# Optimization experiments

Measured on AMD Instinct MI355X. Metric: run time of the kernel, lower is better.

The kernel has to match this reference:

```python
import jax, jax.numpy as jnp
import numpy as np

H = 12        # num attention heads
W = 256       # one-sided window (attention_window // 2)
NEG = -1e9    # additive mask value


def setup_inputs() -> dict:
    key = jax.random.key(0)
    ks = jax.random.split(key, 6)
    B, S, D = 2, 4096, 768
    inp = {
        "hidden_states": jax.random.normal(ks[0], (B, S, D), dtype=jnp.float32),
        "attention_mask": jnp.zeros((B, S), dtype=jnp.float32),
        "Wq": jax.random.normal(ks[1], (D, D), dtype=jnp.float32) * 0.02,
        "bq": jnp.zeros((D,), dtype=jnp.float32),
        "Wk": jax.random.normal(ks[2], (D, D), dtype=jnp.float32) * 0.02,
        "bk": jnp.zeros((D,), dtype=jnp.float32),
        "Wv": jax.random.normal(ks[3], (D, D), dtype=jnp.float32) * 0.02,
        "bv": jnp.zeros((D,), dtype=jnp.float32),
        "Wo": jax.random.normal(ks[4], (D, D), dtype=jnp.float32) * 0.02,
        "bo": jnp.zeros((D,), dtype=jnp.float32),
    }
    return inp


def _sliding_window_attn(hidden_states, attention_mask, Wq, bq, Wk, bk, Wv, bv, Wo, bo):
    B, S, D = hidden_states.shape
    dh = D // H
    b = W                 # chunk size == one-sided window
    nb = S // b           # number of chunks (S must be multiple of W)

    # projections; Longformer scales the query by 1/sqrt(d_head)
    q = (hidden_states @ Wq.T + bq) / jnp.sqrt(jnp.float32(dh))
    k = hidden_states @ Wk.T + bk
    v = hidden_states @ Wv.T + bv

    # [B, H, S, dh]
    q = q.reshape(B, S, H, dh).transpose(0, 2, 1, 3)
    k = k.reshape(B, S, H, dh).transpose(0, 2, 1, 3)
    v = v.reshape(B, S, H, dh).transpose(0, 2, 1, 3)

    # chunk queries: [B, H, nb, b, dh]
    qb = q.reshape(B, H, nb, b, dh)

    # pad K/V by one chunk on each side, gather 3 consecutive chunks per query chunk
    kp = jnp.pad(k, ((0, 0), (0, 0), (b, b), (0, 0)))
    vp = jnp.pad(v, ((0, 0), (0, 0), (b, b), (0, 0)))
    idx = jnp.arange(nb)[:, None] * b + jnp.arange(3 * b)[None, :]  # [nb, 3b] into padded seq
    kw = kp[:, :, idx]  # [B, H, nb, 3b, dh]
    vw = vp[:, :, idx]  # [B, H, nb, 3b, dh]

    # banded scores: [B, H, nb, b, 3b]
    scores = jnp.einsum("bhnqd,bhnkd->bhnqk", qb, kw)

    # band mask: query at local pos qi (global n*b+qi) vs key at local pos ki
    # (global n*b + ki - b); relative offset = ki - b - qi, keep |offset| <= W
    rel = jnp.arange(3 * b)[None, :] - b - jnp.arange(b)[:, None]      # [b, 3b]
    band = jnp.abs(rel) <= W
    # sequence-boundary mask: key global position must lie in [0, S)
    kpos = idx - b                                                      # [nb, 3b]
    inbounds = (kpos >= 0) & (kpos < S)
    valid = band[None, :, :] & inbounds[:, None, :]                     # [nb, b, 3b]

    # key padding bias from attention_mask (wrapper passes attention_mask * -1)
    neg_mask = attention_mask * -1.0                                    # [B, S]
    mp = jnp.pad(neg_mask, ((0, 0), (b, b)))
    key_bias = mp[:, idx]                                               # [B, nb, 3b]

    scores = scores + key_bias[:, None, :, None, :]
    scores = jnp.where(valid[None, None], scores, NEG)

    probs = jax.nn.softmax(scores, axis=-1)
    ctx = jnp.einsum("bhnqk,bhnkd->bhnqd", probs, vw)                   # [B, H, nb, b, dh]
    ctx = ctx.reshape(B, H, S, dh).transpose(0, 2, 1, 3).reshape(B, S, D)

    return ctx @ Wo.T + bo


def reference(hidden_states, attention_mask, Wq, bq, Wk, bk, Wv, bv, Wo, bo):
    return _sliding_window_attn(hidden_states, attention_mask,
                                Wq, bq, Wk, bk, Wv, bv, Wo, bo)
```

## Files before the change

### kernel.cpp

```cpp
#include <hip/hip_runtime.h>
#include <hip/hip_bf16.h>
#include <stdint.h>

#define NH 12
#define DH 64
#define SEQ 4096
#define DM 768
#define NEGV -1e9f
#define LOG2E 1.4426950408889634f
#define QSCALE 0.1803368801111601f

using bf16x8 = __attribute__((ext_vector_type(8))) short;
using f32x4  = __attribute__((ext_vector_type(4))) float;

static __device__ __forceinline__ short f2bf(float f) {
  unsigned u = __builtin_bit_cast(unsigned, f);
  u += 0x7fffu + ((u >> 16) & 1u);
  return (short)(u >> 16);
}

static __device__ __forceinline__ unsigned pack2bf(float lo, float hi) {
  unsigned a = __builtin_bit_cast(unsigned, lo);
  a += 0x7fffu + ((a >> 16) & 1u);
  unsigned b = __builtin_bit_cast(unsigned, hi);
  b += 0x7fffu + ((b >> 16) & 1u);
  return (a >> 16) | (b & 0xffff0000u);
}

static __device__ __forceinline__ void gload16(const void* g, void* l) {
  __builtin_amdgcn_global_load_lds(
      (const __attribute__((address_space(1))) unsigned*)g,
      (__attribute__((address_space(3))) unsigned*)l, 16, 0, 0);
}

static __device__ __forceinline__ f32x4 mfma16(bf16x8 a, bf16x8 b, f32x4 c) {
  return __builtin_amdgcn_mfma_f32_16x16x32_bf16(a, b, c, 0, 0, 0);
}

__global__ __launch_bounds__(256) void cvt_x(const float* __restrict__ X,
                                             short* __restrict__ Xb, int n4) {
  int i = blockIdx.x * 256 + threadIdx.x;
  if (i >= n4) return;
  float4 v = ((const float4*)X)[i];
  short4 o; o.x = f2bf(v.x); o.y = f2bf(v.y); o.z = f2bf(v.z); o.w = f2bf(v.w);
  ((short4*)Xb)[i] = o;
}

__global__ __launch_bounds__(256) void cvt_w(
    const float* __restrict__ Wq, const float* __restrict__ Wk,
    const float* __restrict__ Wv, const float* __restrict__ Wo,
    short* __restrict__ Wqkv, short* __restrict__ Wob) {
  int i = blockIdx.x * 256 + threadIdx.x;
  const int n1 = 2304 * 768 / 4;
  if (i < n1) {
    int e = i * 4;
    int row = e / 768;
    const float* src;
    float sc = 1.0f;
    if (row < 768)       { src = Wq + e; sc = QSCALE; }
    else if (row < 1536) { src = Wk + e - 768 * 768; }
    else                 { src = Wv + e - 1536 * 768; }
    float4 v = *(const float4*)src;
    short4 o; o.x = f2bf(v.x * sc); o.y = f2bf(v.y * sc);
    o.z = f2bf(v.z * sc); o.w = f2bf(v.w * sc);
    ((short4*)Wqkv)[i] = o;
  } else {
    int j = i - n1;
    if (j >= 768 * 768 / 4) return;
    float4 v = ((const float4*)Wo)[j];
    short4 o; o.x = f2bf(v.x); o.y = f2bf(v.y); o.z = f2bf(v.z); o.w = f2bf(v.w);
    ((short4*)Wob)[j] = o;
  }
}

__global__ __launch_bounds__(256) void gemm_qkv(
    const short* __restrict__ Xb, const short* __restrict__ Wqkv,
    const float* __restrict__ bq, const float* __restrict__ bk,
    const float* __restrict__ bv,
    short* __restrict__ qO, short* __restrict__ kO, short* __restrict__ vT) {
  __shared__ __align__(16) short sm[128 * 132];
  short* As = sm;
  short* Bs = sm + 4096;
  const int tid = threadIdx.x, lane = tid & 63, wid = tid >> 6;
  const int m0 = blockIdx.x * 128, n0 = blockIdx.y * 128;
  const int wr = (wid >> 1) * 64, wc = (wid & 1) * 64;
  const int K = 768;
  const short* Ag = Xb + (m0 + (tid >> 2)) * K + ((tid & 3) << 3);
  const short* Bg = Wqkv + (n0 + (tid >> 2)) * K + ((tid & 3) << 3);
  short* Al = As + tid * 8;
  short* Bl = Bs + tid * 8;
  f32x4 acc[4][4] = {};
  for (int kt = 0; kt < K; kt += 32) {
    __syncthreads();
    gload16(Ag + kt, Al);
    gload16(Ag + kt + 64 * K, Al + 2048);
    gload16(Bg + kt, Bl);
    gload16(Bg + kt + 64 * K, Bl + 2048);
    __syncthreads();
    bf16x8 a[4], b[4];
#pragma unroll
    for (int mi = 0; mi < 4; ++mi)
      a[mi] = *(const bf16x8*)&As[(wr + mi * 16 + (lane & 15)) * 32 + ((lane >> 4) << 3)];
#pragma unroll
    for (int ni = 0; ni < 4; ++ni)
      b[ni] = *(const bf16x8*)&Bs[(wc + ni * 16 + (lane & 15)) * 32 + ((lane >> 4) << 3)];
#pragma unroll
    for (int mi = 0; mi < 4; ++mi)
#pragma unroll
      for (int ni = 0; ni < 4; ++ni)
        acc[mi][ni] = mfma16(a[mi], b[ni], acc[mi][ni]);
  }
  const int src = n0 / 768;
  const int bb = m0 >> 12;
  const int s0 = m0 & (SEQ - 1);
  const int nloc = n0 % 768;
  float bias[4];
#pragma unroll
  for (int ni = 0; ni < 4; ++ni) {
    int c = wc + ni * 16 + (lane & 15);
    bias[ni] = (src == 0) ? bq[nloc + c] * QSCALE
             : (src == 1) ? bk[nloc + c] : bv[nloc + c];
  }
  __syncthreads();
  if (src < 2) {
#pragma unroll
    for (int mi = 0; mi < 4; ++mi)
#pragma unroll
      for (int ni = 0; ni < 4; ++ni) {
        int row = wr + mi * 16 + ((lane >> 4) << 2);
        int col = wc + ni * 16 + (lane & 15);
#pragma unroll
        for (int r = 0; r < 4; ++r)
          sm[(row + r) * 132 + col] = f2bf(acc[mi][ni][r] + bias[ni]);
      }
    __syncthreads();
    short* dst = (src == 0) ? qO : kO;
    for (int u = tid; u < 8192; u += 256) {
      int r = u >> 6, cp = (u & 63) << 1;
      unsigned val = *(const unsigned*)&sm[r * 132 + cp];
      int c = nloc + cp;
      int h = c >> 6, d = c & 63;
      *(unsigned*)&dst[(((bb * NH + h) * SEQ) + s0 + r) * DH + d] = val;
    }
  } else {
#pragma unroll
    for (int mi = 0; mi < 4; ++mi)
#pragma unroll
      for (int ni = 0; ni < 4; ++ni) {
        int row = wr + mi * 16 + ((lane >> 4) << 2);
        int col = wc + ni * 16 + (lane & 15);
        short4 pk;
        pk.x = f2bf(acc[mi][ni][0] + bias[ni]);
        pk.y = f2bf(acc[mi][ni][1] + bias[ni]);
        pk.z = f2bf(acc[mi][ni][2] + bias[ni]);
        pk.w = f2bf(acc[mi][ni][3] + bias[ni]);
        *(short4*)&sm[col * 132 + row] = pk;
      }
    __syncthreads();
    for (int u = tid; u < 8192; u += 256) {
      int cc = u >> 6, rp = (u & 63) << 1;
      unsigned val = *(const unsigned*)&sm[cc * 132 + rp];
      int c = nloc + cc;
      int h = c >> 6, d = c & 63;
      *(unsigned*)&vT[(((bb * NH + h) * DH) + d) * SEQ + s0 + rp] = val;
    }
  }
}

__global__ __launch_bounds__(512, 4) void attn(
    const short* __restrict__ qI, const short* __restrict__ kI,
    const short* __restrict__ vT, const float* __restrict__ amask,
    short* __restrict__ ctx) {
  __shared__ __align__(16) short Ks[128 * 64];
  __shared__ __align__(16) short Vs[64 * 128];
  __shared__ __align__(16) short Ps[8][16 * 132];
  const int tid = threadIdx.x, lane = tid & 63, wid = tid >> 6;
  const int vb_id = (blockIdx.x & 7) * 96 + (blockIdx.x >> 3);
  const int strip = vb_id & 31;
  const int hh = (vb_id >> 5) % 12;
  const int bb = vb_id / 384;
  const int s0 = strip * 128;
  const int n = s0 >> 8;
  const int i0 = s0 & 255;
  const int bh = bb * NH + hh;
  const int m = lane & 15, hq = lane >> 4;
  const int swz = m & 7;
  const int iw = i0 + (wid << 4);

  const short* qbase = qI + ((size_t)(bh * SEQ) + s0 + (wid << 4)) * DH;
  const bf16x8 aq0 = *(const bf16x8*)(qbase + m * DH + (hq << 3));
  const bf16x8 aq1 = *(const bf16x8*)(qbase + m * DH + 32 + (hq << 3));

  const int kb_s0 = m * 64 + ((hq ^ swz) << 3);
  const int kb_s1 = m * 64 + (((hq + 4) ^ swz) << 3);
  const int vk0 = m * 128 + ((hq ^ swz) << 3);
  const int vk1 = m * 128 + (((hq + 4) ^ swz) << 3);
  const int vk2 = m * 128 + (((hq + 8) ^ swz) << 3);
  const int vk3 = m * 128 + (((hq + 12) ^ swz) << 3);
  short* Pw = Ps[wid];
  const int pwr = m * 132;

  const int e0 = tid * 8, e1 = tid * 8 + 4096;
  const int kj0 = e0 >> 6, kj1 = e1 >> 6;
  const int ksrc0 = kj0 * DH + ((((e0 >> 3) & 7) ^ (kj0 & 7)) << 3);
  const int ksrc1 = kj1 * DH + ((((e1 >> 3) & 7) ^ (kj1 & 7)) << 3);
  const int vd0 = e0 >> 7, vd1 = e1 >> 7;
  const int vsrc0 = vd0 * SEQ + ((((e0 >> 3) & 15) ^ (vd0 & 7)) << 3);
  const int vsrc1 = vd1 * SEQ + ((((e1 >> 3) & 15) ^ (vd1 & 7)) << 3);

  const short* kg0 = kI + (size_t)bh * SEQ * DH;
  const short* vg0 = vT + (size_t)bh * DH * SEQ;
  const float* mk0 = amask + bb * SEQ + (hq << 2);

  f32x4 acc[4] = {};
  float mrow = -1e30f, lrow = 0.f;

#pragma unroll 1
  for (int c = 0; c < 6; ++c) {
    const int j0 = c << 7;
    const int kpos0 = ((n - 1) << 8) + j0;
    if (kpos0 < 0 || kpos0 >= SEQ) continue;
    if (j0 + 127 < i0 || j0 > i0 + 639) continue;

    __syncthreads();
    {
      const short* kb = kg0 + (size_t)kpos0 * DH;
      gload16(kb + ksrc0, (short*)Ks + e0);
      gload16(kb + ksrc1, (short*)Ks + e1);
      const short* vbp = vg0 + kpos0;
      gload16(vbp + vsrc0, (short*)Vs + e0);
      gload16(vbp + vsrc1, (short*)Vs + e1);
    }
    __syncthreads();

    f32x4 sc[8];
    __builtin_amdgcn_s_setprio(1);
#pragma unroll
    for (int jt = 0; jt < 8; ++jt) {
      bf16x8 k0 = *(const bf16x8*)(Ks + jt * 1024 + kb_s0);
      bf16x8 k1 = *(const bf16x8*)(Ks + jt * 1024 + kb_s1);
      f32x4 z = {};
      z = mfma16(k0, aq0, z);
      z = mfma16(k1, aq1, z);
      sc[jt] = z;
    }
    __builtin_amdgcn_s_setprio(0);

    const float* mp = mk0 + kpos0;
    float mn = mrow;
    const bool interior = (j0 >= iw + 15) && (j0 <= iw + 385);
    if (interior) {
#pragma unroll
      for (int jt = 0; jt < 8; ++jt) {
        float4 b4 = *(const float4*)(mp + jt * 16);
#pragma unroll
        for (int r = 0; r < 4; ++r) {
          float s = fmaf(-LOG2E, (&b4.x)[r], sc[jt][r]);
          sc[jt][r] = s;
          mn = fmaxf(mn, s);
        }
      }
    } else {
      const int iq = iw + m;
#pragma unroll
      for (int jt = 0; jt < 8; ++jt) {
        float4 b4 = *(const float4*)(mp + jt * 16);
        const int jb = j0 + jt * 16 + (hq << 2);
#pragma unroll
        for (int r = 0; r < 4; ++r) {
          int j = jb + r;
          float s = fmaf(-LOG2E, (&b4.x)[r], sc[jt][r]);
          s = (j >= iq && j <= iq + 512) ? s : NEGV;
          sc[jt][r] = s;
          mn = fmaxf(mn, s);
        }
      }
    }
    mn = fmaxf(mn, __shfl_xor(mn, 16));
    mn = fmaxf(mn, __shfl_xor(mn, 32));

    float l0 = 0.f;
#pragma unroll
    for (int jt = 0; jt < 8; ++jt) {
      float p0 = exp2f(sc[jt][0] - mn);
      float p1 = exp2f(sc[jt][1] - mn);
      float p2 = exp2f(sc[jt][2] - mn);
      float p3 = exp2f(sc[jt][3] - mn);
      l0 += (p0 + p1) + (p2 + p3);
      uint2 u;
      u.x = pack2bf(p0, p1);
      u.y = pack2bf(p2, p3);
      *(uint2*)(Pw + pwr + jt * 16 + (hq << 2)) = u;
    }
    l0 += __shfl_xor(l0, 16);
    l0 += __shfl_xor(l0, 32);
    const float scl = exp2f(mrow - mn);
    lrow = lrow * scl + l0;
    mrow = mn;
    const float s0r = __shfl(scl, (hq << 2) + 0);
    const float s1r = __shfl(scl, (hq << 2) + 1);
    const float s2r = __shfl(scl, (hq << 2) + 2);
    const float s3r = __shfl(scl, (hq << 2) + 3);
#pragma unroll
    for (int nt = 0; nt < 4; ++nt) {
      acc[nt][0] *= s0r; acc[nt][1] *= s1r;
      acc[nt][2] *= s2r; acc[nt][3] *= s3r;
    }

    asm volatile("s_waitcnt lgkmcnt(0)" ::: "memory");
    __builtin_amdgcn_sched_barrier(0);

    __builtin_amdgcn_s_setprio(1);
#pragma unroll
    for (int ks = 0; ks < 4; ++ks) {
      bf16x8 pa = *(const bf16x8*)(Pw + pwr + ks * 32 + (hq << 3));
      const int vkk = (ks == 0) ? vk0 : (ks == 1) ? vk1 : (ks == 2) ? vk2 : vk3;
#pragma unroll
      for (int nt = 0; nt < 4; ++nt) {
        bf16x8 vv = *(const bf16x8*)(Vs + nt * 2048 + vkk);
        acc[nt] = mfma16(pa, vv, acc[nt]);
      }
    }
    __builtin_amdgcn_s_setprio(0);
  }

  const float inv = 1.0f / lrow;
  const float i0r = __shfl(inv, (hq << 2) + 0);
  const float i1r = __shfl(inv, (hq << 2) + 1);
  const float i2r = __shfl(inv, (hq << 2) + 2);
  const float i3r = __shfl(inv, (hq << 2) + 3);
#pragma unroll
  for (int nt = 0; nt < 4; ++nt) {
    Pw[((hq << 2) + 0) * 72 + nt * 16 + m] = f2bf(acc[nt][0] * i0r);
    Pw[((hq << 2) + 1) * 72 + nt * 16 + m] = f2bf(acc[nt][1] * i1r);
    Pw[((hq << 2) + 2) * 72 + nt * 16 + m] = f2bf(acc[nt][2] * i2r);
    Pw[((hq << 2) + 3) * 72 + nt * 16 + m] = f2bf(acc[nt][3] * i3r);
  }
  asm volatile("s_waitcnt lgkmcnt(0)" ::: "memory");
  __builtin_amdgcn_sched_barrier(0);
#pragma unroll
  for (int it = 0; it < 2; ++it) {
    int row = it * 8 + (lane >> 3);
    bf16x8 val = *(const bf16x8*)(Pw + row * 72 + ((lane & 7) << 3));
    *(bf16x8*)(ctx + ((size_t)(bb * SEQ) + s0 + (wid << 4) + row) * DM +
               hh * DH + ((lane & 7) << 3)) = val;
  }
}

__global__ __launch_bounds__(256) void gemm_out(
    const short* __restrict__ Cb, const short* __restrict__ Wob,
    const float* __restrict__ bo, float* __restrict__ out) {
  __shared__ __align__(16) short As[128 * 32];
  __shared__ __align__(16) short Bs[128 * 32];
  const int tid = threadIdx.x, lane = tid & 63, wid = tid >> 6;
  const int m0 = blockIdx.x * 128, n0 = blockIdx.y * 128;
  const int wr = (wid >> 1) * 64, wc = (wid & 1) * 64;
  const int K = 768;
  const short* Ag = Cb + (m0 + (tid >> 2)) * K + ((tid & 3) << 3);
  const short* Bg = Wob + (n0 + (tid >> 2)) * K + ((tid & 3) << 3);
  short* Al = As + tid * 8;
  short* Bl = Bs + tid * 8;
  f32x4 acc[4][4] = {};
  for (int kt = 0; kt < K; kt += 32) {
    __syncthreads();
    gload16(Ag + kt, Al);
    gload16(Ag + kt + 64 * K, Al + 2048);
    gload16(Bg + kt, Bl);
    gload16(Bg + kt + 64 * K, Bl + 2048);
    __syncthreads();
    bf16x8 a[4], b[4];
#pragma unroll
    for (int mi = 0; mi < 4; ++mi)
      a[mi] = *(const bf16x8*)&As[(wr + mi * 16 + (lane & 15)) * 32 + ((lane >> 4) << 3)];
#pragma unroll
    for (int ni = 0; ni < 4; ++ni)
      b[ni] = *(const bf16x8*)&Bs[(wc + ni * 16 + (lane & 15)) * 32 + ((lane >> 4) << 3)];
#pragma unroll
    for (int mi = 0; mi < 4; ++mi)
#pragma unroll
      for (int ni = 0; ni < 4; ++ni)
        acc[mi][ni] = mfma16(a[mi], b[ni], acc[mi][ni]);
  }
  float bias[4];
#pragma unroll
  for (int ni = 0; ni < 4; ++ni)
    bias[ni] = bo[n0 + wc + ni * 16 + (lane & 15)];
#pragma unroll
  for (int mi = 0; mi < 4; ++mi)
#pragma unroll
    for (int ni = 0; ni < 4; ++ni) {
      int row = m0 + wr + mi * 16 + ((lane >> 4) << 2);
      int col = n0 + wc + ni * 16 + (lane & 15);
#pragma unroll
      for (int r = 0; r < 4; ++r)
        out[(row + r) * DM + col] = acc[mi][ni][r] + bias[ni];
    }
}

extern "C" void kernel_launch(void* const* d_in, const int* in_sizes, int n_in,
                              void* d_out, int out_size, void* d_ws, size_t ws_size,
                              hipStream_t stream) {
  (void)in_sizes; (void)n_in; (void)out_size; (void)ws_size;
  const float* hs    = (const float*)d_in[0];
  const float* amask = (const float*)d_in[1];
  const float* Wq = (const float*)d_in[2];
  const float* bq = (const float*)d_in[3];
  const float* Wk = (const float*)d_in[4];
  const float* bk = (const float*)d_in[5];
  const float* Wv = (const float*)d_in[6];
  const float* bv = (const float*)d_in[7];
  const float* Wo = (const float*)d_in[8];
  const float* bo = (const float*)d_in[9];
  float* out = (float*)d_out;
  char* ws = (char*)d_ws;
  short* Xb   = (short*)(ws);
  short* Wqkv = (short*)(ws + 12582912);
  short* Wob  = (short*)(ws + 16121856);
  short* qB   = (short*)(ws + 17301504);
  short* kB   = (short*)(ws + 29884416);
  short* vTB  = (short*)(ws + 42467328);
  short* ctx  = Xb;

  cvt_x<<<dim3(6144), dim3(256), 0, stream>>>(hs, Xb, 8192 * 768 / 4);
  cvt_w<<<dim3(2304), dim3(256), 0, stream>>>(Wq, Wk, Wv, Wo, Wqkv, Wob);
  gemm_qkv<<<dim3(64, 18), dim3(256), 0, stream>>>(Xb, Wqkv, bq, bk, bv, qB, kB, vTB);
  attn<<<dim3(768), dim3(512), 0, stream>>>(qB, kB, vTB, amask, ctx);
  gemm_out<<<dim3(64, 6), dim3(256), 0, stream>>>(ctx, Wob, bo, out);
}
```

Measured before the change: 150.4 us.

## Pipeline both GEMMs with 4-stage LDS ring, XOR swizzle, and XCD-aware tile mapping

Replaces the single-buffered load/sync/compute loop in the QKV and output GEMMs with a four-slot LDS ring that keeps three k-tiles of global-to-LDS loads in flight. It uses explicit vmcnt waits and one barrier per iteration, and raises MFMA priority with s_setprio. The LDS column layout is XOR-swizzled to reduce bank conflicts on fragment reads. The 2D grid is flattened with an XCD-aware block-to-tile mapping so that neighbouring M tiles land on the same XCD for L2 reuse. The cost is more LDS per block (64KB), which may lower occupancy, plus fragile manual waitcnt accounting.

```diff
diff --git a/kernel.cpp b/kernel.cpp
--- a/kernel.cpp
+++ b/kernel.cpp
@@ -36,6 +36,12 @@
 static __device__ __forceinline__ f32x4 mfma16(bf16x8 a, bf16x8 b, f32x4 c) {
   return __builtin_amdgcn_mfma_f32_16x16x32_bf16(a, b, c, 0, 0, 0);
 }
+
+#define SBAR() __builtin_amdgcn_sched_barrier(0)
+#define WAIT8() asm volatile("s_waitcnt vmcnt(8)" ::: "memory")
+#define WAIT4() asm volatile("s_waitcnt vmcnt(4)" ::: "memory")
+#define WAIT0() asm volatile("s_waitcnt vmcnt(0)" ::: "memory")
+#define HBAR() __builtin_amdgcn_s_barrier()
 
 __global__ __launch_bounds__(256) void cvt_x(const float* __restrict__ X,
                                              short* __restrict__ Xb, int n4) {
@@ -73,54 +79,80 @@
   }
 }
 
+#define GEMM_PIPELINE(SM, AG, BG, ACC, LANE, WR, WC)                           \
+  {                                                                            \
+    const int l15 = (LANE) & 15, gw = (LANE) >> 4;                             \
+    const int s_ = (l15 >> 1) & 3;                                             \
+    const int fcol = ((gw ^ s_) << 3);                                         \
+    const int NT = 24;                                             \
+    auto stage = [&](int t) {                                                  \
+      short* ab = (SM) + ((t & 3) << 12);                                      \
+      short* bb = (SM) + 16384 + ((t & 3) << 12);                              \
+      int kt = t << 5;                                                         \
+      gload16((AG) + kt, ab + ldst);                                           \
+      gload16((AG) + kt + 64 * 768, ab + ldst + 2048);                         \
+      gload16((BG) + kt, bb + ldst);                                           \
+      gload16((BG) + kt + 64 * 768, bb + ldst + 2048);                         \
+    };                                                                         \
+    auto compute = [&](int t) {                                                \
+      const short* ab = (SM) + ((t & 3) << 12);                                \
+      const short* bb = (SM) + 16384 + ((t & 3) << 12);                        \
+      bf16x8 af[4], bf[4];                                                     \
+      _Pragma("unroll") for (int mi = 0; mi < 4; ++mi)                         \
+          af[mi] = *(const bf16x8*)(ab + ((WR) + mi * 16 + l15) * 32 + fcol);  \
+      _Pragma("unroll") for (int ni = 0; ni < 4; ++ni)                         \
+          bf[ni] = *(const bf16x8*)(bb + ((WC) + ni * 16 + l15) * 32 + fcol);  \
+      __builtin_amdgcn_s_setprio(1);                                           \
+      _Pragma("unroll") for (int mi = 0; mi < 4; ++mi)                         \
+          _Pragma("unroll") for (int ni = 0; ni < 4; ++ni)                     \
+              ACC[mi][ni] = mfma16(af[mi], bf[ni], ACC[mi][ni]);               \
+      __builtin_amdgcn_s_setprio(0);                                           \
+    };                                                                         \
+    stage(0); stage(1); stage(2);                                              \
+    SBAR();                                                                    \
+    _Pragma("unroll 1") for (int i = 0; i < NT - 3; ++i) {                     \
+      SBAR(); WAIT8(); HBAR(); SBAR();                                         \
+      stage(i + 3);                                                            \
+      SBAR();                                                                  \
+      compute(i);                                                              \
+    }                                                                          \
+    SBAR(); WAIT8(); HBAR(); SBAR(); compute(NT - 3);                          \
+    SBAR(); WAIT4(); HBAR(); SBAR(); compute(NT - 2);                          \
+    SBAR(); WAIT0(); HBAR(); SBAR(); compute(NT - 1);                          \
+  }
+
 __global__ __launch_bounds__(256) void gemm_qkv(
     const short* __restrict__ Xb, const short* __restrict__ Wqkv,
     const float* __restrict__ bq, const float* __restrict__ bk,
     const float* __restrict__ bv,
     short* __restrict__ qO, short* __restrict__ kO, short* __restrict__ vT) {
-  __shared__ __align__(16) short sm[128 * 132];
-  short* As = sm;
-  short* Bs = sm + 4096;
+  __shared__ __align__(16) short sm[32768];
   const int tid = threadIdx.x, lane = tid & 63, wid = tid >> 6;
-  const int m0 = blockIdx.x * 128, n0 = blockIdx.y * 128;
+  const int xcd = blockIdx.x & 7, kk = blockIdx.x >> 3;
+  const int m0 = (xcd * 8 + (kk & 7)) * 128;
+  const int n0 = (kk >> 3) * 128;
   const int wr = (wid >> 1) * 64, wc = (wid & 1) * 64;
-  const int K = 768;
-  const short* Ag = Xb + (m0 + (tid >> 2)) * K + ((tid & 3) << 3);
-  const short* Bg = Wqkv + (n0 + (tid >> 2)) * K + ((tid & 3) << 3);
-  short* Al = As + tid * 8;
-  short* Bl = Bs + tid * 8;
+  const int srow = tid >> 2;
+  const int scol = (((tid & 3) ^ ((srow >> 1) & 3)) << 3);
+  const short* Ag = Xb + (m0 + srow) * 768 + scol;
+  const short* Bg = Wqkv + (n0 + srow) * 768 + scol;
+  const int ldst = tid * 8;
+
+  const int src = n0 / 768;
+  const int nloc = n0 % 768;
+  float bias[4];
+#pragma unroll
+  for (int ni = 0; ni < 4; ++ni) {
+    int c = nloc + wc + ni * 16 + (lane & 15);
+    bias[ni] = (src == 0) ? bq[c] * QSCALE : (src == 1) ? bk[c] : bv[c];
+  }
+  WAIT0(); SBAR();
+
   f32x4 acc[4][4] = {};
-  for (int kt = 0; kt < K; kt += 32) {
-    __syncthreads();
-    gload16(Ag + kt, Al);
-    gload16(Ag + kt + 64 * K, Al + 2048);
-    gload16(Bg + kt, Bl);
-    gload16(Bg + kt + 64 * K, Bl + 2048);
-    __syncthreads();
-    bf16x8 a[4], b[4];
-#pragma unroll
-    for (int mi = 0; mi < 4; ++mi)
-      a[mi] = *(const bf16x8*)&As[(wr + mi * 16 + (lane & 15)) * 32 + ((lane >> 4) << 3)];
-#pragma unroll
-    for (int ni = 0; ni < 4; ++ni)
-      b[ni] = *(const bf16x8*)&Bs[(wc + ni * 16 + (lane & 15)) * 32 + ((lane >> 4) << 3)];
-#pragma unroll
-    for (int mi = 0; mi < 4; ++mi)
-#pragma unroll
-      for (int ni = 0; ni < 4; ++ni)
-        acc[mi][ni] = mfma16(a[mi], b[ni], acc[mi][ni]);
-  }
-  const int src = n0 / 768;
+  GEMM_PIPELINE(sm, Ag, Bg, acc, lane, wr, wc);
+
   const int bb = m0 >> 12;
   const int s0 = m0 & (SEQ - 1);
-  const int nloc = n0 % 768;
-  float bias[4];
-#pragma unroll
-  for (int ni = 0; ni < 4; ++ni) {
-    int c = wc + ni * 16 + (lane & 15);
-    bias[ni] = (src == 0) ? bq[nloc + c] * QSCALE
-             : (src == 1) ? bk[nloc + c] : bv[nloc + c];
-  }
   __syncthreads();
   if (src < 2) {
 #pragma unroll
@@ -350,41 +382,27 @@
 __global__ __launch_bounds__(256) void gemm_out(
     const short* __restrict__ Cb, const short* __restrict__ Wob,
     const float* __restrict__ bo, float* __restrict__ out) {
-  __shared__ __align__(16) short As[128 * 32];
-  __shared__ __align__(16) short Bs[128 * 32];
+  __shared__ __align__(16) short sm[32768];
   const int tid = threadIdx.x, lane = tid & 63, wid = tid >> 6;
-  const int m0 = blockIdx.x * 128, n0 = blockIdx.y * 128;
+  const int xcd = blockIdx.x & 7, kk = blockIdx.x >> 3;
+  const int m0 = (xcd * 8 + (kk & 7)) * 128;
+  const int n0 = (kk >> 3) * 128;
   const int wr = (wid >> 1) * 64, wc = (wid & 1) * 64;
-  const int K = 768;
-  const short* Ag = Cb + (m0 + (tid >> 2)) * K + ((tid & 3) << 3);
-  const short* Bg = Wob + (n0 + (tid >> 2)) * K + ((tid & 3) << 3);
-  short* Al = As + tid * 8;
-  short* Bl = Bs + tid * 8;
-  f32x4 acc[4][4] = {};
-  for (int kt = 0; kt < K; kt += 32) {
-    __syncthreads();
-    gload16(Ag + kt, Al);
-    gload16(Ag + kt + 64 * K, Al + 2048);
-    gload16(Bg + kt, Bl);
-    gload16(Bg + kt + 64 * K, Bl + 2048);
-    __syncthreads();
-    bf16x8 a[4], b[4];
-#pragma unroll
-    for (int mi = 0; mi < 4; ++mi)
-      a[mi] = *(const bf16x8*)&As[(wr + mi * 16 + (lane & 15)) * 32 + ((lane >> 4) << 3)];
-#pragma unroll
-    for (int ni = 0; ni < 4; ++ni)
-      b[ni] = *(const bf16x8*)&Bs[(wc + ni * 16 + (lane & 15)) * 32 + ((lane >> 4) << 3)];
-#pragma unroll
-    for (int mi = 0; mi < 4; ++mi)
-#pragma unroll
-      for (int ni = 0; ni < 4; ++ni)
-        acc[mi][ni] = mfma16(a[mi], b[ni], acc[mi][ni]);
-  }
+  const int srow = tid >> 2;
+  const int scol = (((tid & 3) ^ ((srow >> 1) & 3)) << 3);
+  const short* Ag = Cb + (m0 + srow) * 768 + scol;
+  const short* Bg = Wob + (n0 + srow) * 768 + scol;
+  const int ldst = tid * 8;
+
   float bias[4];
 #pragma unroll
   for (int ni = 0; ni < 4; ++ni)
     bias[ni] = bo[n0 + wc + ni * 16 + (lane & 15)];
+  WAIT0(); SBAR();
+
+  f32x4 acc[4][4] = {};
+  GEMM_PIPELINE(sm, Ag, Bg, acc, lane, wr, wc);
+
 #pragma unroll
   for (int mi = 0; mi < 4; ++mi)
 #pragma unroll
@@ -423,7 +441,7 @@
 
   cvt_x<<<dim3(6144), dim3(256), 0, stream>>>(hs, Xb, 8192 * 768 / 4);
   cvt_w<<<dim3(2304), dim3(256), 0, stream>>>(Wq, Wk, Wv, Wo, Wqkv, Wob);
-  gemm_qkv<<<dim3(64, 18), dim3(256), 0, stream>>>(Xb, Wqkv, bq, bk, bv, qB, kB, vTB);
+  gemm_qkv<<<dim3(1152), dim3(256), 0, stream>>>(Xb, Wqkv, bq, bk, bv, qB, kB, vTB);
   attn<<<dim3(768), dim3(512), 0, stream>>>(qB, kB, vTB, amask, ctx);
-  gemm_out<<<dim3(64, 6), dim3(256), 0, stream>>>(ctx, Wob, bo, out);
-}
+  gemm_out<<<dim3(384), dim3(256), 0, stream>>>(ctx, Wob, bo, out);
+}
```

Measured after the change: 134.8 us. -10.4%, faster.
